# Kernel tuning notes

Hardware: AMD Instinct MI355X
Metric: run time of the kernel (lower is better)

Reference implementation:

```python
import math
import jax, jax.numpy as jnp
import numpy as np

D_MODEL = 1024
N_HEADS = 16
D_K = D_MODEL // N_HEADS


def _build_neighbours(n_heads):
    # Mirrors LatticeMultiHeadAttention._build_neighbours for a (4,4)-style lattice.
    side = int(math.sqrt(n_heads))
    cols = side + 1 if side * side < n_heads else side
    positions = [divmod(i, cols) for i in range(n_heads)]
    pos_map = {p: j for j, p in enumerate(positions)}
    nb_idx = np.full((n_heads, 8), -1, dtype=np.int64)
    nb_w = np.zeros((n_heads, 8), dtype=np.float32)
    for i, (r, c) in enumerate(positions):
        k = 0
        for dr in (-1, 0, 1):
            for dc in (-1, 0, 1):
                if dr == 0 and dc == 0:
                    continue
                j = pos_map.get((r + dr, c + dc))
                if j is not None and k < 8:
                    nb_idx[i, k] = j
                    nb_w[i, k] = math.exp(-math.hypot(dr, dc))
                    k += 1
    return nb_idx, nb_w


def _phase_biases(coupling):
    # Sequential Kuramoto phase update: head h uses neighbor phases already
    # updated for heads < h (exactly as the torch per-head loop mutates buffers).
    H = coupling.shape[0]
    nb_idx, nb_w = _build_neighbours(H)
    phases = [jnp.asarray(0.0, coupling.dtype) for _ in range(H)]
    two_pi = 2.0 * math.pi
    for h in range(H):
        force = jnp.asarray(0.0, coupling.dtype)
        for k in range(8):
            j = int(nb_idx[h, k])
            if j >= 0:
                force = force + jnp.asarray(nb_w[h, k], coupling.dtype) * jnp.sin(phases[j] - phases[h])
        intrinsic = 1.0 + 0.1 * h
        new_phase = (phases[h] + 0.01 * (intrinsic + coupling[h] * force)) % two_pi
        phases[h] = new_phase
    return 0.1 * jnp.cos(jnp.stack(phases))  # [H] per-head scalar bias


def setup_inputs() -> dict:
    key = jax.random.key(0)
    ks = jax.random.split(key, 9)
    B, L = 2, 2048
    std = 0.02
    return {
        "query": jax.random.normal(ks[0], (B, L, D_MODEL), jnp.float32),
        "key": jax.random.normal(ks[1], (B, L, D_MODEL), jnp.float32),
        "value": jax.random.normal(ks[2], (B, L, D_MODEL), jnp.float32),
        "Wq": std * jax.random.normal(ks[3], (N_HEADS, D_MODEL, D_K), jnp.float32),
        "Wk": std * jax.random.normal(ks[4], (N_HEADS, D_MODEL, D_K), jnp.float32),
        "Wv": std * jax.random.normal(ks[5], (N_HEADS, D_MODEL, D_K), jnp.float32),
        "out_w": std * jax.random.normal(ks[6], (D_MODEL, D_MODEL), jnp.float32),
        "out_b": jnp.zeros((D_MODEL,), jnp.float32),
        "coupling": 0.1 * jnp.ones((N_HEADS,), jnp.float32),
    }


def reference(query, key, value, Wq, Wk, Wv, out_w, out_b, coupling):
    d_k = Wq.shape[-1]
    Q = jnp.einsum("bld,hdk->bhlk", query, Wq)
    K = jnp.einsum("bld,hdk->bhlk", key, Wk)
    V = jnp.einsum("bld,hdk->bhlk", value, Wv)
    scale = jnp.asarray(math.sqrt(float(d_k)), query.dtype)
    scores = jnp.einsum("bhlk,bhmk->bhlm", Q, K) / scale
    bias = _phase_biases(coupling)  # [H]
    scores = scores + bias[None, :, None, None]
    attn = jax.nn.softmax(scores, axis=-1)
    ctx = jnp.einsum("bhlm,bhmk->bhlk", attn, V)
    B, H, L, _ = ctx.shape
    out = ctx.transpose(0, 2, 1, 3).reshape(B, L, H * d_k)  # concat heads
    return out @ out_w + out_b
```

## Files before the change

### kernel.cpp

```cpp
#include <hip/hip_runtime.h>
#include <cstdint>

typedef uint16_t u16;
typedef __attribute__((ext_vector_type(8))) short bf16x8;
typedef __attribute__((ext_vector_type(4))) short bf16x4;
typedef __attribute__((ext_vector_type(4))) float f32x4;

#define QSCALE 0.18033688011112042f

struct Ptr3 { const float* a; const float* b; const float* c; };

__device__ __forceinline__ u16 f2bf(float x) {
  union { float f; uint32_t u; } v; v.f = x;
  uint32_t r = (v.u + 0x7fffu + ((v.u >> 16) & 1u)) >> 16;
  return (u16)r;
}

__device__ __forceinline__ void async16(void* lds, const void* g) {
  __builtin_amdgcn_global_load_lds((const __attribute__((address_space(1))) void*)g,
                                   (__attribute__((address_space(3))) void*)lds, 16, 0, 0);
}

__global__ __launch_bounds__(256) void k_cast3(Ptr3 in, u16* __restrict__ out) {
  const int z = blockIdx.y;
  const float* p = z == 0 ? in.a : (z == 1 ? in.b : in.c);
  int i = blockIdx.x * 256 + threadIdx.x;
  float4 v = ((const float4*)p)[i];
  bf16x4 o;
  o[0] = (short)f2bf(v.x); o[1] = (short)f2bf(v.y);
  o[2] = (short)f2bf(v.z); o[3] = (short)f2bf(v.w);
  *(bf16x4*)(out + (long)z * 4194304 + (long)i * 4) = o;
}

__global__ __launch_bounds__(256) void k_transpose_w(Ptr3 w, u16* __restrict__ out) {
  __shared__ u16 tile[64 * 72];
  const int t = threadIdx.x;
  const int z = blockIdx.z;
  const float* in = (z < 16) ? w.a : (z < 32 ? w.b : w.c);
  const long in_base = (long)(z & 15) * 65536;
  const long out_base = (long)z * 65536;
  const int r0 = blockIdx.x * 64;
  for (int e = t; e < 4096; e += 256) {
    int rr = e >> 6, cc = e & 63;
    tile[rr * 72 + cc] = f2bf(in[in_base + (long)(r0 + rr) * 64 + cc]);
  }
  __syncthreads();
  for (int s = t; s < 512; s += 256) {
    int cc = s >> 3, r8 = (s & 7) << 3;
    bf16x8 p;
    #pragma unroll
    for (int j = 0; j < 8; ++j) p[j] = (short)tile[(r8 + j) * 72 + cc];
    *(bf16x8*)(out + out_base + (long)cc * 1024 + r0 + r8) = p;
  }
}

__global__ __launch_bounds__(256) void k_transpose_bf16(const void* __restrict__ in,
                                                        int in_is_f32, u16* __restrict__ out,
                                                        int rstride, int R, int sph,
                                                        long slab_lo, long slab_hi) {
  __shared__ u16 tile[64 * 72];
  const int t = threadIdx.x;
  const long z = blockIdx.z;
  const long in_base = (z / sph) * slab_hi + (z % sph) * slab_lo;
  const long out_base = z * (long)R * (long)(gridDim.y * 64);
  const int r0 = blockIdx.x * 64, c0 = blockIdx.y * 64;
  for (int e = t; e < 4096; e += 256) {
    int rr = e >> 6, cc = e & 63;
    long src = in_base + (long)(r0 + rr) * rstride + c0 + cc;
    u16 w = in_is_f32 ? f2bf(((const float*)in)[src]) : ((const u16*)in)[src];
    tile[rr * 72 + cc] = w;
  }
  __syncthreads();
  for (int s = t; s < 512; s += 256) {
    int cc = s >> 3, r8 = (s & 7) << 3;
    bf16x8 p;
    #pragma unroll
    for (int j = 0; j < 8; ++j) p[j] = (short)tile[(r8 + j) * 72 + cc];
    *(bf16x8*)(out + out_base + (long)(c0 + cc) * R + r0 + r8) = p;
  }
}

__global__ __launch_bounds__(256) void k_gemm_qkv(const u16* __restrict__ A0,
                                                  const u16* __restrict__ B0,
                                                  u16* __restrict__ C0, float scale0) {
  __shared__ __align__(16) u16 As[128 * 32];
  __shared__ __align__(16) u16 Bs[128 * 32];
  const int z = blockIdx.z;
  const u16* A = A0 + (long)z * 4194304;
  const u16* Bt = B0 + (long)z * 1048576;
  u16* C = C0 + (long)z * 4194304;
  const float scale = z ? 1.0f : scale0;
  const int t = threadIdx.x, lane = t & 63, quad = lane >> 4, l16 = lane & 15;
  const int wave = t >> 6, wy = wave >> 1, wx = wave & 1;
  const int m0 = blockIdx.y * 128, n0 = blockIdx.x * 128;
  const int wbase = t & 192;
  f32x4 acc[4][4] = {};
  for (int k0 = 0; k0 < 1024; k0 += 32) {
    __syncthreads();
    #pragma unroll
    for (int i = 0; i < 2; ++i) {
      int sb = i * 256 + wbase;
      int s = sb + lane;
      int row = s >> 2, c = s & 3;
      async16(As + sb * 8, A + (long)(m0 + row) * 1024 + k0 + c * 8);
      async16(Bs + sb * 8, Bt + (long)(n0 + row) * 1024 + k0 + c * 8);
    }
    __syncthreads();
    bf16x8 af[4], bfr[4];
    #pragma unroll
    for (int mt = 0; mt < 4; ++mt)
      af[mt] = *(const bf16x8*)(As + (wy * 64 + mt * 16 + l16) * 32 + quad * 8);
    #pragma unroll
    for (int nt = 0; nt < 4; ++nt)
      bfr[nt] = *(const bf16x8*)(Bs + (wx * 64 + nt * 16 + l16) * 32 + quad * 8);
    #pragma unroll
    for (int mt = 0; mt < 4; ++mt)
      #pragma unroll
      for (int nt = 0; nt < 4; ++nt)
        acc[mt][nt] = __builtin_amdgcn_mfma_f32_16x16x32_bf16(af[mt], bfr[nt], acc[mt][nt], 0, 0, 0);
  }
  #pragma unroll
  for (int mt = 0; mt < 4; ++mt)
    #pragma unroll
    for (int nt = 0; nt < 4; ++nt) {
      int col = n0 + wx * 64 + nt * 16 + l16;
      #pragma unroll
      for (int r = 0; r < 4; ++r) {
        int row = m0 + wy * 64 + mt * 16 + quad * 4 + r;
        C[(long)row * 1024 + col] = f2bf(acc[mt][nt][r] * scale);
      }
    }
}

__global__ __launch_bounds__(256) void k_gemm_out(const u16* __restrict__ A,
                                                  const u16* __restrict__ Bt,
                                                  float* __restrict__ C,
                                                  const float* __restrict__ bias) {
  __shared__ __align__(16) u16 As[128 * 32];
  __shared__ __align__(16) u16 Bs[64 * 32];
  const int t = threadIdx.x, lane = t & 63, quad = lane >> 4, l16 = lane & 15;
  const int wave = t >> 6;
  const int m0 = blockIdx.y * 128, n0 = blockIdx.x * 64;
  const int wbase = t & 192;
  f32x4 acc[2][4] = {};
  for (int k0 = 0; k0 < 1024; k0 += 32) {
    __syncthreads();
    #pragma unroll
    for (int i = 0; i < 2; ++i) {
      int sb = i * 256 + wbase;
      int s = sb + lane;
      int row = s >> 2, c = s & 3;
      async16(As + sb * 8, A + (long)(m0 + row) * 1024 + k0 + c * 8);
    }
    {
      int s = t;
      int row = s >> 2, c = s & 3;
      async16(Bs + wbase * 8, Bt + (long)(n0 + row) * 1024 + k0 + c * 8);
    }
    __syncthreads();
    bf16x8 af[2], bfr[4];
    #pragma unroll
    for (int mt = 0; mt < 2; ++mt)
      af[mt] = *(const bf16x8*)(As + (wave * 32 + mt * 16 + l16) * 32 + quad * 8);
    #pragma unroll
    for (int nt = 0; nt < 4; ++nt)
      bfr[nt] = *(const bf16x8*)(Bs + (nt * 16 + l16) * 32 + quad * 8);
    #pragma unroll
    for (int mt = 0; mt < 2; ++mt)
      #pragma unroll
      for (int nt = 0; nt < 4; ++nt)
        acc[mt][nt] = __builtin_amdgcn_mfma_f32_16x16x32_bf16(af[mt], bfr[nt], acc[mt][nt], 0, 0, 0);
  }
  #pragma unroll
  for (int mt = 0; mt < 2; ++mt)
    #pragma unroll
    for (int nt = 0; nt < 4; ++nt) {
      int col = n0 + nt * 16 + l16;
      #pragma unroll
      for (int r = 0; r < 4; ++r) {
        int row = m0 + wave * 32 + mt * 16 + quad * 4 + r;
        C[(long)row * 1024 + col] = acc[mt][nt][r] + bias[col];
      }
    }
}

__global__ __launch_bounds__(512, 2) void k_flash(const u16* __restrict__ Qp,
                                                  const u16* __restrict__ Kp,
                                                  const u16* __restrict__ Vt,
                                                  u16* __restrict__ ctx) {
  __shared__ __align__(16) u16 qs[256 * 64];
  __shared__ __align__(16) u16 ks[64 * 72];
  __shared__ __align__(16) u16 vs[64 * 72];
  const int t = threadIdx.x, lane = t & 63, quad = lane >> 4, l16 = lane & 15;
  const int wave = t >> 6;
  const int bh = blockIdx.x & 31, b = bh >> 4, h = bh & 15;
  const int q0 = (blockIdx.x >> 5) * 256;
  const long gkbase = (long)b * 2097152 + h * 64;
  const long gvbase = (long)bh * 131072;
  const int srow = t >> 3, sc = t & 7;

  {
    long gq = (long)(b * 2048 + q0) * 1024 + h * 64;
    #pragma unroll
    for (int i = 0; i < 4; ++i) {
      int s = i * 512 + t;
      int row = s >> 3, pos = s & 7, c = pos ^ (row & 7);
      async16(qs + (long)s * 8, Qp + gq + (long)row * 1024 + c * 8);
    }
  }
  bf16x8 kreg = *(const bf16x8*)(Kp + gkbase + (long)srow * 1024 + sc * 8);
  bf16x8 vreg = *(const bf16x8*)(Vt + gvbase + (long)srow * 2048 + sc * 8);
  __syncthreads();

  bf16x8 qf[2][2];
  #pragma unroll
  for (int msub = 0; msub < 2; ++msub)
    #pragma unroll
    for (int kh = 0; kh < 2; ++kh) {
      int m = wave * 32 + msub * 16 + l16;
      int pos = (kh * 4 + quad) ^ (m & 7);
      qf[msub][kh] = *(const bf16x8*)(qs + m * 64 + pos * 8);
    }
  *(bf16x8*)(ks + srow * 72 + sc * 8) = kreg;
  *(bf16x8*)(vs + srow * 72 + sc * 8) = vreg;
  __syncthreads();

  u16* pw = qs + wave * 1152;

  float lsum[2][4] = {};
  f32x4 o[2][4] = {};

  for (int kt = 0; kt < 32; ++kt) {
    if (kt < 31) {
      int kv0 = (kt + 1) * 64;
      kreg = *(const bf16x8*)(Kp + gkbase + (long)(kv0 + srow) * 1024 + sc * 8);
      vreg = *(const bf16x8*)(Vt + gvbase + kv0 + (long)srow * 2048 + sc * 8);
    }

    bf16x8 kf[4][2], vf[4][2];
    #pragma unroll
    for (int nt = 0; nt < 4; ++nt)
      #pragma unroll
      for (int kh = 0; kh < 2; ++kh) {
        kf[nt][kh] = *(const bf16x8*)(ks + (nt * 16 + l16) * 72 + kh * 32 + quad * 8);
        vf[nt][kh] = *(const bf16x8*)(vs + (nt * 16 + l16) * 72 + kh * 32 + quad * 8);
      }

    #pragma unroll
    for (int msub = 0; msub < 2; ++msub) {
      #pragma unroll
      for (int nt = 0; nt < 4; ++nt) {
        f32x4 a = {};
        #pragma unroll
        for (int kh = 0; kh < 2; ++kh)
          a = __builtin_amdgcn_mfma_f32_16x16x32_bf16(qf[msub][kh], kf[nt][kh], a, 0, 0, 0);
        #pragma unroll
        for (int r = 0; r < 4; ++r) {
          float e = __builtin_amdgcn_exp2f(a[r]);
          lsum[msub][r] += e;
          pw[(quad * 4 + r) * 72 + nt * 16 + l16] = f2bf(e);
        }
      }
      #pragma unroll
      for (int kh = 0; kh < 2; ++kh) {
        bf16x8 pa = *(const bf16x8*)(pw + l16 * 72 + kh * 32 + quad * 8);
        #pragma unroll
        for (int nt = 0; nt < 4; ++nt)
          o[msub][nt] = __builtin_amdgcn_mfma_f32_16x16x32_bf16(pa, vf[nt][kh], o[msub][nt], 0, 0, 0);
      }
    }

    __syncthreads();
    if (kt < 31) {
      *(bf16x8*)(ks + srow * 72 + sc * 8) = kreg;
      *(bf16x8*)(vs + srow * 72 + sc * 8) = vreg;
    }
    __syncthreads();
  }

  #pragma unroll
  for (int msub = 0; msub < 2; ++msub)
    #pragma unroll
    for (int r = 0; r < 4; ++r) {
      float l = lsum[msub][r];
      #pragma unroll
      for (int d = 1; d < 16; d <<= 1) l += __shfl_xor(l, d);
      lsum[msub][r] = 1.0f / l;
    }
  #pragma unroll
  for (int msub = 0; msub < 2; ++msub)
    #pragma unroll
    for (int nt = 0; nt < 4; ++nt)
      #pragma unroll
      for (int r = 0; r < 4; ++r) {
        int q = q0 + wave * 32 + msub * 16 + quad * 4 + r;
        long idx = (long)(b * 2048 + q) * 1024 + h * 64 + nt * 16 + l16;
        ctx[idx] = f2bf(o[msub][nt][r] * lsum[msub][r]);
      }
}

extern "C" void kernel_launch(void* const* d_in, const int* in_sizes, int n_in,
                              void* d_out, int out_size, void* d_ws, size_t ws_size,
                              hipStream_t stream) {
  const float* query = (const float*)d_in[0];
  const float* key   = (const float*)d_in[1];
  const float* value = (const float*)d_in[2];
  const float* Wq    = (const float*)d_in[3];
  const float* Wk    = (const float*)d_in[4];
  const float* Wv    = (const float*)d_in[5];
  const float* out_w = (const float*)d_in[6];
  const float* out_b = (const float*)d_in[7];
  float* out = (float*)d_out;

  char* ws = (char*)d_ws;
  size_t off = 0;
  auto alloc = [&](size_t bytes) {
    void* p = ws + off;
    off += (bytes + 255) & ~(size_t)255;
    return p;
  };
  u16* qb  = (u16*)alloc(4096L * 1024 * 2);
  u16* kb  = (u16*)alloc(4096L * 1024 * 2);
  u16* vb  = (u16*)alloc(4096L * 1024 * 2);
  u16* wtq = (u16*)alloc(1024L * 1024 * 2);
  u16* wtk = (u16*)alloc(1024L * 1024 * 2);
  u16* wtv = (u16*)alloc(1024L * 1024 * 2);
  u16* wto = (u16*)alloc(1024L * 1024 * 2);
  u16* Qp  = (u16*)alloc(4096L * 1024 * 2);
  u16* Kp  = (u16*)alloc(4096L * 1024 * 2);
  u16* Vp  = (u16*)alloc(4096L * 1024 * 2);
  u16* Vtb = (u16*)alloc(4096L * 1024 * 2);
  u16* ctx = qb;
  (void)kb; (void)vb; (void)wtk; (void)wtv; (void)Kp; (void)Vp;

  k_cast3<<<dim3(4096, 3), 256, 0, stream>>>(Ptr3{query, key, value}, qb);

  k_transpose_w<<<dim3(16, 1, 48), 256, 0, stream>>>(Ptr3{Wq, Wk, Wv}, wtq);
  k_transpose_bf16<<<dim3(16, 16, 1), 256, 0, stream>>>(out_w, 1, wto, 1024, 1024, 1, 0L, 0L);

  k_gemm_qkv<<<dim3(8, 32, 3), 256, 0, stream>>>(qb, wtq, Qp, QSCALE);

  k_transpose_bf16<<<dim3(32, 1, 32), 256, 0, stream>>>(Vp, 0, Vtb, 1024, 2048, 16, 64L, 2097152L);

  k_flash<<<256, 512, 0, stream>>>(Qp, Kp, Vtb, ctx);

  k_gemm_out<<<dim3(16, 32), 256, 0, stream>>>(ctx, wto, out, out_b);
}
```

Before: 250.4 us.

## Fuse fp32 cast into QKV GEMM, register-prefetch GEMMs, shrink flash tile

The separate fp32-to-bf16 cast kernel is removed; the QKV GEMM now loads fp32 activations directly and converts them while staging into padded LDS. Both GEMMs swap direct global-to-LDS async loads for register prefetch of the next k-tile, and their LDS rows are padded. The flash kernel halves the query tile to 128 rows per block, doubling the grid and raising the occupancy hint, and the transpose kernels use an odd LDS stride. The changes aim to cut a full pass of activation traffic and increase parallelism, at the cost of twice the fp32 A reads in the GEMM and more K/V reloads in flash.

```diff
diff --git a/kernel.cpp b/kernel.cpp
--- a/kernel.cpp
+++ b/kernel.cpp
@@ -16,24 +16,17 @@
   return (u16)r;
 }
 
-__device__ __forceinline__ void async16(void* lds, const void* g) {
-  __builtin_amdgcn_global_load_lds((const __attribute__((address_space(1))) void*)g,
-                                   (__attribute__((address_space(3))) void*)lds, 16, 0, 0);
-}
-
-__global__ __launch_bounds__(256) void k_cast3(Ptr3 in, u16* __restrict__ out) {
-  const int z = blockIdx.y;
-  const float* p = z == 0 ? in.a : (z == 1 ? in.b : in.c);
-  int i = blockIdx.x * 256 + threadIdx.x;
-  float4 v = ((const float4*)p)[i];
-  bf16x4 o;
-  o[0] = (short)f2bf(v.x); o[1] = (short)f2bf(v.y);
-  o[2] = (short)f2bf(v.z); o[3] = (short)f2bf(v.w);
-  *(bf16x4*)(out + (long)z * 4194304 + (long)i * 4) = o;
+__device__ __forceinline__ bf16x8 cvt8(f32x4 lo, f32x4 hi) {
+  bf16x8 o;
+  o[0] = (short)f2bf(lo[0]); o[1] = (short)f2bf(lo[1]);
+  o[2] = (short)f2bf(lo[2]); o[3] = (short)f2bf(lo[3]);
+  o[4] = (short)f2bf(hi[0]); o[5] = (short)f2bf(hi[1]);
+  o[6] = (short)f2bf(hi[2]); o[7] = (short)f2bf(hi[3]);
+  return o;
 }
 
 __global__ __launch_bounds__(256) void k_transpose_w(Ptr3 w, u16* __restrict__ out) {
-  __shared__ u16 tile[64 * 72];
+  __shared__ u16 tile[64 * 65];
   const int t = threadIdx.x;
   const int z = blockIdx.z;
   const float* in = (z < 16) ? w.a : (z < 32 ? w.b : w.c);
@@ -42,14 +35,14 @@
   const int r0 = blockIdx.x * 64;
   for (int e = t; e < 4096; e += 256) {
     int rr = e >> 6, cc = e & 63;
-    tile[rr * 72 + cc] = f2bf(in[in_base + (long)(r0 + rr) * 64 + cc]);
+    tile[rr * 65 + cc] = f2bf(in[in_base + (long)(r0 + rr) * 64 + cc]);
   }
   __syncthreads();
   for (int s = t; s < 512; s += 256) {
     int cc = s >> 3, r8 = (s & 7) << 3;
     bf16x8 p;
     #pragma unroll
-    for (int j = 0; j < 8; ++j) p[j] = (short)tile[(r8 + j) * 72 + cc];
+    for (int j = 0; j < 8; ++j) p[j] = (short)tile[(r8 + j) * 65 + cc];
     *(bf16x8*)(out + out_base + (long)cc * 1024 + r0 + r8) = p;
   }
 }
@@ -58,7 +51,7 @@
                                                         int in_is_f32, u16* __restrict__ out,
                                                         int rstride, int R, int sph,
                                                         long slab_lo, long slab_hi) {
-  __shared__ u16 tile[64 * 72];
+  __shared__ u16 tile[64 * 65];
   const int t = threadIdx.x;
   const long z = blockIdx.z;
   const long in_base = (z / sph) * slab_hi + (z % sph) * slab_lo;
@@ -68,56 +61,74 @@
     int rr = e >> 6, cc = e & 63;
     long src = in_base + (long)(r0 + rr) * rstride + c0 + cc;
     u16 w = in_is_f32 ? f2bf(((const float*)in)[src]) : ((const u16*)in)[src];
-    tile[rr * 72 + cc] = w;
+    tile[rr * 65 + cc] = w;
   }
   __syncthreads();
   for (int s = t; s < 512; s += 256) {
     int cc = s >> 3, r8 = (s & 7) << 3;
     bf16x8 p;
     #pragma unroll
-    for (int j = 0; j < 8; ++j) p[j] = (short)tile[(r8 + j) * 72 + cc];
+    for (int j = 0; j < 8; ++j) p[j] = (short)tile[(r8 + j) * 65 + cc];
     *(bf16x8*)(out + out_base + (long)(c0 + cc) * R + r0 + r8) = p;
   }
 }
 
-__global__ __launch_bounds__(256) void k_gemm_qkv(const u16* __restrict__ A0,
-                                                  const u16* __restrict__ B0,
-                                                  u16* __restrict__ C0, float scale0) {
-  __shared__ __align__(16) u16 As[128 * 32];
-  __shared__ __align__(16) u16 Bs[128 * 32];
+__global__ __launch_bounds__(256, 3) void k_gemm_qkv(Ptr3 Af, const u16* __restrict__ B0,
+                                                     u16* __restrict__ C0, float scale0) {
+  __shared__ __align__(16) u16 As[128 * 34];
+  __shared__ __align__(16) u16 Bs[128 * 34];
   const int z = blockIdx.z;
-  const u16* A = A0 + (long)z * 4194304;
+  const float* A = z == 0 ? Af.a : (z == 1 ? Af.b : Af.c);
   const u16* Bt = B0 + (long)z * 1048576;
   u16* C = C0 + (long)z * 4194304;
   const float scale = z ? 1.0f : scale0;
   const int t = threadIdx.x, lane = t & 63, quad = lane >> 4, l16 = lane & 15;
   const int wave = t >> 6, wy = wave >> 1, wx = wave & 1;
   const int m0 = blockIdx.y * 128, n0 = blockIdx.x * 128;
-  const int wbase = t & 192;
+  const int srow = t >> 1, shalf = t & 1;
+  const float* aptr = A + (long)(m0 + srow) * 1024 + shalf * 16;
+  const u16* bptr = Bt + (long)(n0 + srow) * 1024 + shalf * 16;
+  u16* asl = As + srow * 34 + shalf * 16;
+  u16* bsl = Bs + srow * 34 + shalf * 16;
+
+  f32x4 ar[4];
+  bf16x8 br[2];
+  auto loadT = [&](int k0) {
+    #pragma unroll
+    for (int i = 0; i < 4; ++i) ar[i] = ((const f32x4*)(aptr + k0))[i];
+    br[0] = ((const bf16x8*)(bptr + k0))[0];
+    br[1] = ((const bf16x8*)(bptr + k0))[1];
+  };
+  auto writeT = [&]() {
+    *(bf16x8*)asl = cvt8(ar[0], ar[1]);
+    *(bf16x8*)(asl + 8) = cvt8(ar[2], ar[3]);
+    *(bf16x8*)bsl = br[0];
+    *(bf16x8*)(bsl + 8) = br[1];
+  };
+
+  loadT(0);
+  writeT();
+  __syncthreads();
+
   f32x4 acc[4][4] = {};
   for (int k0 = 0; k0 < 1024; k0 += 32) {
-    __syncthreads();
-    #pragma unroll
-    for (int i = 0; i < 2; ++i) {
-      int sb = i * 256 + wbase;
-      int s = sb + lane;
-      int row = s >> 2, c = s & 3;
-      async16(As + sb * 8, A + (long)(m0 + row) * 1024 + k0 + c * 8);
-      async16(Bs + sb * 8, Bt + (long)(n0 + row) * 1024 + k0 + c * 8);
-    }
-    __syncthreads();
+    const bool pre = (k0 + 32) < 1024;
+    if (pre) loadT(k0 + 32);
     bf16x8 af[4], bfr[4];
     #pragma unroll
     for (int mt = 0; mt < 4; ++mt)
-      af[mt] = *(const bf16x8*)(As + (wy * 64 + mt * 16 + l16) * 32 + quad * 8);
+      af[mt] = *(const bf16x8*)(As + (wy * 64 + mt * 16 + l16) * 34 + quad * 8);
     #pragma unroll
     for (int nt = 0; nt < 4; ++nt)
-      bfr[nt] = *(const bf16x8*)(Bs + (wx * 64 + nt * 16 + l16) * 32 + quad * 8);
+      bfr[nt] = *(const bf16x8*)(Bs + (wx * 64 + nt * 16 + l16) * 34 + quad * 8);
     #pragma unroll
     for (int mt = 0; mt < 4; ++mt)
       #pragma unroll
       for (int nt = 0; nt < 4; ++nt)
         acc[mt][nt] = __builtin_amdgcn_mfma_f32_16x16x32_bf16(af[mt], bfr[nt], acc[mt][nt], 0, 0, 0);
+    __syncthreads();
+    if (pre) writeT();
+    __syncthreads();
   }
   #pragma unroll
   for (int mt = 0; mt < 4; ++mt)
@@ -132,44 +143,54 @@
     }
 }
 
-__global__ __launch_bounds__(256) void k_gemm_out(const u16* __restrict__ A,
-                                                  const u16* __restrict__ Bt,
-                                                  float* __restrict__ C,
-                                                  const float* __restrict__ bias) {
-  __shared__ __align__(16) u16 As[128 * 32];
-  __shared__ __align__(16) u16 Bs[64 * 32];
+__global__ __launch_bounds__(256, 2) void k_gemm_out(const u16* __restrict__ A,
+                                                     const u16* __restrict__ Bt,
+                                                     float* __restrict__ C,
+                                                     const float* __restrict__ bias) {
+  __shared__ __align__(16) u16 As[128 * 34];
+  __shared__ __align__(16) u16 Bs[64 * 34];
   const int t = threadIdx.x, lane = t & 63, quad = lane >> 4, l16 = lane & 15;
   const int wave = t >> 6;
   const int m0 = blockIdx.y * 128, n0 = blockIdx.x * 64;
-  const int wbase = t & 192;
+  const int ar0 = t >> 2, ac0 = t & 3;
+  const int ar1 = (t + 256) >> 2, ac1 = t & 3;
+  const int brow = t >> 2, bc = t & 3;
+
+  bf16x8 areg[2], breg;
+  auto loadT = [&](int k0) {
+    areg[0] = *(const bf16x8*)(A + (long)(m0 + ar0) * 1024 + k0 + ac0 * 8);
+    areg[1] = *(const bf16x8*)(A + (long)(m0 + ar1) * 1024 + k0 + ac1 * 8);
+    breg = *(const bf16x8*)(Bt + (long)(n0 + brow) * 1024 + k0 + bc * 8);
+  };
+  auto writeT = [&]() {
+    *(bf16x8*)(As + ar0 * 34 + ac0 * 8) = areg[0];
+    *(bf16x8*)(As + ar1 * 34 + ac1 * 8) = areg[1];
+    *(bf16x8*)(Bs + brow * 34 + bc * 8) = breg;
+  };
+
+  loadT(0);
+  writeT();
+  __syncthreads();
+
   f32x4 acc[2][4] = {};
   for (int k0 = 0; k0 < 1024; k0 += 32) {
-    __syncthreads();
-    #pragma unroll
-    for (int i = 0; i < 2; ++i) {
-      int sb = i * 256 + wbase;
-      int s = sb + lane;
-      int row = s >> 2, c = s & 3;
-      async16(As + sb * 8, A + (long)(m0 + row) * 1024 + k0 + c * 8);
-    }
-    {
-      int s = t;
-      int row = s >> 2, c = s & 3;
-      async16(Bs + wbase * 8, Bt + (long)(n0 + row) * 1024 + k0 + c * 8);
-    }
-    __syncthreads();
+    const bool pre = (k0 + 32) < 1024;
+    if (pre) loadT(k0 + 32);
     bf16x8 af[2], bfr[4];
     #pragma unroll
     for (int mt = 0; mt < 2; ++mt)
-      af[mt] = *(const bf16x8*)(As + (wave * 32 + mt * 16 + l16) * 32 + quad * 8);
+      af[mt] = *(const bf16x8*)(As + (wave * 32 + mt * 16 + l16) * 34 + quad * 8);
     #pragma unroll
     for (int nt = 0; nt < 4; ++nt)
-      bfr[nt] = *(const bf16x8*)(Bs + (nt * 16 + l16) * 32 + quad * 8);
+      bfr[nt] = *(const bf16x8*)(Bs + (nt * 16 + l16) * 34 + quad * 8);
     #pragma unroll
     for (int mt = 0; mt < 2; ++mt)
       #pragma unroll
       for (int nt = 0; nt < 4; ++nt)
         acc[mt][nt] = __builtin_amdgcn_mfma_f32_16x16x32_bf16(af[mt], bfr[nt], acc[mt][nt], 0, 0, 0);
+    __syncthreads();
+    if (pre) writeT();
+    __syncthreads();
   }
   #pragma unroll
   for (int mt = 0; mt < 2; ++mt)
@@ -184,51 +205,40 @@
     }
 }
 
-__global__ __launch_bounds__(512, 2) void k_flash(const u16* __restrict__ Qp,
+__global__ __launch_bounds__(512, 4) void k_flash(const u16* __restrict__ Qp,
                                                   const u16* __restrict__ Kp,
                                                   const u16* __restrict__ Vt,
                                                   u16* __restrict__ ctx) {
-  __shared__ __align__(16) u16 qs[256 * 64];
-  __shared__ __align__(16) u16 ks[64 * 72];
-  __shared__ __align__(16) u16 vs[64 * 72];
+  __shared__ __align__(16) u16 qs[128 * 68];
+  __shared__ __align__(16) u16 ks[64 * 68];
+  __shared__ __align__(16) u16 vs[64 * 68];
   const int t = threadIdx.x, lane = t & 63, quad = lane >> 4, l16 = lane & 15;
   const int wave = t >> 6;
   const int bh = blockIdx.x & 31, b = bh >> 4, h = bh & 15;
-  const int q0 = (blockIdx.x >> 5) * 256;
+  const int q0 = (blockIdx.x >> 5) * 128;
   const long gkbase = (long)b * 2097152 + h * 64;
   const long gvbase = (long)bh * 131072;
   const int srow = t >> 3, sc = t & 7;
 
-  {
-    long gq = (long)(b * 2048 + q0) * 1024 + h * 64;
-    #pragma unroll
-    for (int i = 0; i < 4; ++i) {
-      int s = i * 512 + t;
-      int row = s >> 3, pos = s & 7, c = pos ^ (row & 7);
-      async16(qs + (long)s * 8, Qp + gq + (long)row * 1024 + c * 8);
-    }
-  }
+  const long gq = (long)(b * 2048 + q0) * 1024 + h * 64;
+  bf16x8 q0r = *(const bf16x8*)(Qp + gq + (long)(t >> 3) * 1024 + (t & 7) * 8);
+  bf16x8 q1r = *(const bf16x8*)(Qp + gq + (long)((t + 512) >> 3) * 1024 + (t & 7) * 8);
   bf16x8 kreg = *(const bf16x8*)(Kp + gkbase + (long)srow * 1024 + sc * 8);
   bf16x8 vreg = *(const bf16x8*)(Vt + gvbase + (long)srow * 2048 + sc * 8);
-  __syncthreads();
-
-  bf16x8 qf[2][2];
-  #pragma unroll
-  for (int msub = 0; msub < 2; ++msub)
-    #pragma unroll
-    for (int kh = 0; kh < 2; ++kh) {
-      int m = wave * 32 + msub * 16 + l16;
-      int pos = (kh * 4 + quad) ^ (m & 7);
-      qf[msub][kh] = *(const bf16x8*)(qs + m * 64 + pos * 8);
-    }
-  *(bf16x8*)(ks + srow * 72 + sc * 8) = kreg;
-  *(bf16x8*)(vs + srow * 72 + sc * 8) = vreg;
-  __syncthreads();
-
-  u16* pw = qs + wave * 1152;
-
-  float lsum[2][4] = {};
-  f32x4 o[2][4] = {};
+  *(bf16x8*)(qs + (t >> 3) * 68 + (t & 7) * 8) = q0r;
+  *(bf16x8*)(qs + ((t + 512) >> 3) * 68 + (t & 7) * 8) = q1r;
+  *(bf16x8*)(ks + srow * 68 + sc * 8) = kreg;
+  *(bf16x8*)(vs + srow * 68 + sc * 8) = vreg;
+  __syncthreads();
+
+  bf16x8 qf[2];
+  #pragma unroll
+  for (int kh = 0; kh < 2; ++kh)
+    qf[kh] = *(const bf16x8*)(qs + (wave * 16 + l16) * 68 + kh * 32 + quad * 8);
+  u16* pw = qs + wave * 16 * 68;
+
+  float lsum[4] = {};
+  f32x4 o[4] = {};
 
   for (int kt = 0; kt < 32; ++kt) {
     if (kt < 31) {
@@ -237,66 +247,55 @@
       vreg = *(const bf16x8*)(Vt + gvbase + kv0 + (long)srow * 2048 + sc * 8);
     }
 
-    bf16x8 kf[4][2], vf[4][2];
-    #pragma unroll
-    for (int nt = 0; nt < 4; ++nt)
+    #pragma unroll
+    for (int nt = 0; nt < 4; ++nt) {
+      f32x4 a = {};
       #pragma unroll
       for (int kh = 0; kh < 2; ++kh) {
-        kf[nt][kh] = *(const bf16x8*)(ks + (nt * 16 + l16) * 72 + kh * 32 + quad * 8);
-        vf[nt][kh] = *(const bf16x8*)(vs + (nt * 16 + l16) * 72 + kh * 32 + quad * 8);
-      }
-
-    #pragma unroll
-    for (int msub = 0; msub < 2; ++msub) {
+        bf16x8 kf = *(const bf16x8*)(ks + (nt * 16 + l16) * 68 + kh * 32 + quad * 8);
+        a = __builtin_amdgcn_mfma_f32_16x16x32_bf16(qf[kh], kf, a, 0, 0, 0);
+      }
+      #pragma unroll
+      for (int r = 0; r < 4; ++r) {
+        float e = __builtin_amdgcn_exp2f(a[r]);
+        lsum[r] += e;
+        pw[(quad * 4 + r) * 68 + nt * 16 + l16] = f2bf(e);
+      }
+    }
+
+    #pragma unroll
+    for (int kh = 0; kh < 2; ++kh) {
+      bf16x8 pa = *(const bf16x8*)(pw + l16 * 68 + kh * 32 + quad * 8);
       #pragma unroll
       for (int nt = 0; nt < 4; ++nt) {
-        f32x4 a = {};
-        #pragma unroll
-        for (int kh = 0; kh < 2; ++kh)
-          a = __builtin_amdgcn_mfma_f32_16x16x32_bf16(qf[msub][kh], kf[nt][kh], a, 0, 0, 0);
-        #pragma unroll
-        for (int r = 0; r < 4; ++r) {
-          float e = __builtin_amdgcn_exp2f(a[r]);
-          lsum[msub][r] += e;
-          pw[(quad * 4 + r) * 72 + nt * 16 + l16] = f2bf(e);
-        }
-      }
-      #pragma unroll
-      for (int kh = 0; kh < 2; ++kh) {
-        bf16x8 pa = *(const bf16x8*)(pw + l16 * 72 + kh * 32 + quad * 8);
-        #pragma unroll
-        for (int nt = 0; nt < 4; ++nt)
-          o[msub][nt] = __builtin_amdgcn_mfma_f32_16x16x32_bf16(pa, vf[nt][kh], o[msub][nt], 0, 0, 0);
+        bf16x8 vf = *(const bf16x8*)(vs + (nt * 16 + l16) * 68 + kh * 32 + quad * 8);
+        o[nt] = __builtin_amdgcn_mfma_f32_16x16x32_bf16(pa, vf, o[nt], 0, 0, 0);
       }
     }
 
     __syncthreads();
     if (kt < 31) {
-      *(bf16x8*)(ks + srow * 72 + sc * 8) = kreg;
-      *(bf16x8*)(vs + srow * 72 + sc * 8) = vreg;
-    }
-    __syncthreads();
-  }
-
-  #pragma unroll
-  for (int msub = 0; msub < 2; ++msub)
+      *(bf16x8*)(ks + srow * 68 + sc * 8) = kreg;
+      *(bf16x8*)(vs + srow * 68 + sc * 8) = vreg;
+    }
+    __syncthreads();
+  }
+
+  #pragma unroll
+  for (int r = 0; r < 4; ++r) {
+    float l = lsum[r];
+    #pragma unroll
+    for (int d = 1; d < 16; d <<= 1) l += __shfl_xor(l, d);
+    lsum[r] = 1.0f / l;
+  }
+  #pragma unroll
+  for (int nt = 0; nt < 4; ++nt)
     #pragma unroll
     for (int r = 0; r < 4; ++r) {
-      float l = lsum[msub][r];
-      #pragma unroll
-      for (int d = 1; d < 16; d <<= 1) l += __shfl_xor(l, d);
-      lsum[msub][r] = 1.0f / l;
-    }
-  #pragma unroll
-  for (int msub = 0; msub < 2; ++msub)
-    #pragma unroll
-    for (int nt = 0; nt < 4; ++nt)
-      #pragma unroll
-      for (int r = 0; r < 4; ++r) {
-        int q = q0 + wave * 32 + msub * 16 + quad * 4 + r;
-        long idx = (long)(b * 2048 + q) * 1024 + h * 64 + nt * 16 + l16;
-        ctx[idx] = f2bf(o[msub][nt][r] * lsum[msub][r]);
-      }
+      int q = q0 + wave * 16 + quad * 4 + r;
+      long idx = (long)(b * 2048 + q) * 1024 + h * 64 + nt * 16 + l16;
+      ctx[idx] = f2bf(o[nt][r] * lsum[r]);
+    }
 }
 
 extern "C" void kernel_launch(void* const* d_in, const int* in_sizes, int n_in,
@@ -319,9 +318,6 @@
     off += (bytes + 255) & ~(size_t)255;
     return p;
   };
-  u16* qb  = (u16*)alloc(4096L * 1024 * 2);
-  u16* kb  = (u16*)alloc(4096L * 1024 * 2);
-  u16* vb  = (u16*)alloc(4096L * 1024 * 2);
   u16* wtq = (u16*)alloc(1024L * 1024 * 2);
   u16* wtk = (u16*)alloc(1024L * 1024 * 2);
   u16* wtv = (u16*)alloc(1024L * 1024 * 2);
@@ -330,19 +326,17 @@
   u16* Kp  = (u16*)alloc(4096L * 1024 * 2);
   u16* Vp  = (u16*)alloc(4096L * 1024 * 2);
   u16* Vtb = (u16*)alloc(4096L * 1024 * 2);
-  u16* ctx = qb;
-  (void)kb; (void)vb; (void)wtk; (void)wtv; (void)Kp; (void)Vp;
-
-  k_cast3<<<dim3(4096, 3), 256, 0, stream>>>(Ptr3{query, key, value}, qb);
+  u16* ctx = (u16*)alloc(4096L * 1024 * 2);
+  (void)wtk; (void)wtv; (void)Kp; (void)Vp;
 
   k_transpose_w<<<dim3(16, 1, 48), 256, 0, stream>>>(Ptr3{Wq, Wk, Wv}, wtq);
   k_transpose_bf16<<<dim3(16, 16, 1), 256, 0, stream>>>(out_w, 1, wto, 1024, 1024, 1, 0L, 0L);
 
-  k_gemm_qkv<<<dim3(8, 32, 3), 256, 0, stream>>>(qb, wtq, Qp, QSCALE);
+  k_gemm_qkv<<<dim3(8, 32, 3), 256, 0, stream>>>(Ptr3{query, key, value}, wtq, Qp, QSCALE);
 
   k_transpose_bf16<<<dim3(32, 1, 32), 256, 0, stream>>>(Vp, 0, Vtb, 1024, 2048, 16, 64L, 2097152L);
 
-  k_flash<<<256, 512, 0, stream>>>(Qp, Kp, Vtb, ctx);
+  k_flash<<<512, 512, 0, stream>>>(Qp, Kp, Vtb, ctx);
 
   k_gemm_out<<<dim3(16, 32), 256, 0, stream>>>(ctx, wto, out, out_b);
 }
```

Result: slower. 303.8 us (+21.3%).
